# Kernel optimization log

Measured on AMD Instinct MI355X. Metric: run time of the kernel, lower is better.

The kernel has to match this reference:

```python
import jax, jax.numpy as jnp
import numpy as np

B, T, DIN, H = 8, 4096, 1024, 2048
INIT_SCALE = 0.1


def setup_inputs() -> dict:
    key = jax.random.key(0)
    ks = jax.random.split(key, 5)
    x = jax.random.normal(ks[0], (B, T, DIN), dtype=jnp.float32)
    Wi = jax.random.normal(ks[1], (H, DIN), dtype=jnp.float32) * INIT_SCALE
    Wg = jax.random.normal(ks[2], (H, DIN), dtype=jnp.float32) * INIT_SCALE
    Wo = jax.random.normal(ks[3], (DIN, H), dtype=jnp.float32) * INIT_SCALE
    log_a = jax.random.normal(ks[4], (H,), dtype=jnp.float32) * INIT_SCALE - 1.0
    bi = jnp.zeros((H,), dtype=jnp.float32)
    bg = jnp.zeros((H,), dtype=jnp.float32)
    bo = jnp.zeros((DIN,), dtype=jnp.float32)
    return {"x": x, "Wi": Wi, "bi": bi, "Wg": Wg, "bg": bg,
            "Wo": Wo, "bo": bo, "log_a": log_a}


def _lru_forward(x, Wi, bi, Wg, bg, Wo, bo, log_a):
    # u, gate: (B, T, H)
    u = jnp.einsum('btd,hd->bth', x, Wi) + bi
    gate = jax.nn.sigmoid(jnp.einsum('btd,hd->bth', x, Wg) + bg)
    a = jax.nn.sigmoid(log_a)  # (H,) diagonal recurrence coefficient

    # diagonal linear recurrence h_t = a*h_{t-1} + u_t, scanned over time
    def step(h, u_t):
        h = a * h + u_t
        return h, h

    u_tbh = jnp.swapaxes(u, 0, 1)  # (T, B, H)
    h0 = jnp.zeros((x.shape[0], log_a.shape[0]), dtype=x.dtype)
    _, h_seq = jax.lax.scan(step, h0, u_tbh)  # (T, B, H)
    h_seq = jnp.swapaxes(h_seq, 0, 1)  # (B, T, H)

    y = jnp.einsum('bth,dh->btd', h_seq * gate, Wo) + bo
    return y


def reference(x, Wi, bi, Wg, bg, Wo, bo, log_a):
    return _lru_forward(x, Wi, bi, Wg, bg, Wo, bo, log_a)
```

## Files before the change

### kernel.cpp

```cpp
#include <hip/hip_runtime.h>
#include <hip/hip_bf16.h>
#include <stdint.h>

using bf16 = __hip_bfloat16;

typedef short bf16x8 __attribute__((ext_vector_type(8)));
typedef float f32x4 __attribute__((ext_vector_type(4)));

#define BM 128
#define BN 128
#define BK 32

__device__ __forceinline__ float bf2f(bf16 x) { return __bfloat162float(x); }
__device__ __forceinline__ bf16 f2bf(float x) { return __float2bfloat16(x); }

__device__ __forceinline__ void async_load16(const bf16* gptr, bf16* lptr) {
    __builtin_amdgcn_global_load_lds(
        (const __attribute__((address_space(1))) void*)gptr,
        (__attribute__((address_space(3))) void*)lptr,
        16, 0, 0);
}

template <int MODE>
__global__ __launch_bounds__(256, 2) void gemm_bt(
    const bf16* __restrict__ A, const bf16* __restrict__ Bt,
    const float* __restrict__ bias, void* __restrict__ Cout,
    int M, int N, int K)
{
    __shared__ bf16 As[BM * BK];
    __shared__ bf16 Bs[BN * BK];

    const int tid  = threadIdx.x;
    const int wid  = tid >> 6;
    const int lane = tid & 63;

    const int m0 = blockIdx.y * BM;
    const int n0 = blockIdx.x * BN;
    const int wm = (wid >> 1) * 64;
    const int wn = (wid & 1) * 64;

    f32x4 acc[4][4];
#pragma unroll
    for (int i = 0; i < 4; ++i)
#pragma unroll
        for (int j = 0; j < 4; ++j)
            acc[i][j] = f32x4{0.f, 0.f, 0.f, 0.f};

    const int ar = lane >> 2;
    const int ac = (lane & 3) * 8;

    const bf16* Abase = A + (size_t)m0 * K;
    const bf16* Bbase = Bt + (size_t)n0 * K;

    const int frow = lane & 15;
    const int fk   = (lane >> 4) * 8;

    for (int k0 = 0; k0 < K; k0 += BK) {
        __syncthreads();
#pragma unroll
        for (int c = 0; c < 2; ++c) {
            const int chunk = wid + 4 * c;
            const int row = chunk * 16 + ar;
            async_load16(Abase + (size_t)row * K + (k0 + ac), &As[chunk * (16 * BK)]);
            async_load16(Bbase + (size_t)row * K + (k0 + ac), &Bs[chunk * (16 * BK)]);
        }
        __syncthreads();

        bf16x8 afrag[4], bfrag[4];
#pragma unroll
        for (int i = 0; i < 4; ++i) {
            afrag[i] = *(const bf16x8*)&As[(wm + 16 * i + frow) * BK + fk];
            bfrag[i] = *(const bf16x8*)&Bs[(wn + 16 * i + frow) * BK + fk];
        }
#pragma unroll
        for (int i = 0; i < 4; ++i)
#pragma unroll
            for (int j = 0; j < 4; ++j)
                acc[i][j] = __builtin_amdgcn_mfma_f32_16x16x32_bf16(
                    afrag[i], bfrag[j], acc[i][j], 0, 0, 0);
    }

    const int crow = (lane >> 4) * 4;
    const int ccol = lane & 15;
#pragma unroll
    for (int i = 0; i < 4; ++i) {
#pragma unroll
        for (int j = 0; j < 4; ++j) {
            const int col = n0 + wn + 16 * j + ccol;
            const float bv = bias[col];
#pragma unroll
            for (int r = 0; r < 4; ++r) {
                const int row = m0 + wm + 16 * i + crow + r;
                float v = acc[i][j][r] + bv;
                if constexpr (MODE == 1) v = 1.f / (1.f + __expf(-v));
                if constexpr (MODE == 2)
                    ((float*)Cout)[(size_t)row * N + col] = v;
                else
                    ((bf16*)Cout)[(size_t)row * N + col] = f2bf(v);
            }
        }
    }
}

#define SCAN_T 4096
#define SCAN_H 2048
#define SCAN_B 8
#define SCAN_L 512
#define SCAN_W 64

__global__ __launch_bounds__(256) void lru_scan(
    const bf16* __restrict__ u, bf16* gs, const float* __restrict__ asig)
{
    const int tid   = blockIdx.x * 256 + threadIdx.x;
    const int h     = tid & (SCAN_H - 1);
    const int rem   = tid >> 11;
    const int b     = rem & (SCAN_B - 1);
    const int chunk = rem >> 3;

    const float a = asig[h];
    const size_t base = (size_t)b * SCAN_T * SCAN_H + h;
    const bf16* up = u + base;
    bf16* gp = gs + base;

    const int t1 = chunk * SCAN_L;
    const int warm0 = (chunk == 0) ? 0 : SCAN_W;

    float hs = 0.f;
    for (int t = t1 - warm0; t < t1; t += 8) {
        float uv[8];
#pragma unroll
        for (int i = 0; i < 8; ++i) uv[i] = bf2f(up[(size_t)(t + i) * SCAN_H]);
#pragma unroll
        for (int i = 0; i < 8; ++i) hs = fmaf(a, hs, uv[i]);
    }
    for (int t = t1; t < t1 + SCAN_L; t += 8) {
        float uv[8], gv[8];
#pragma unroll
        for (int i = 0; i < 8; ++i) {
            uv[i] = bf2f(up[(size_t)(t + i) * SCAN_H]);
            gv[i] = bf2f(gp[(size_t)(t + i) * SCAN_H]);
        }
#pragma unroll
        for (int i = 0; i < 8; ++i) {
            hs = fmaf(a, hs, uv[i]);
            gp[(size_t)(t + i) * SCAN_H] = f2bf(hs * gv[i]);
        }
    }
}

__global__ void cvt_f32_bf16_x4(const float* __restrict__ in,
                                bf16* __restrict__ out, int n4)
{
    const int i = blockIdx.x * blockDim.x + threadIdx.x;
    if (i >= n4) return;
    const float4 v = ((const float4*)in)[i];
    bf16 h[4] __attribute__((aligned(8)));
    h[0] = f2bf(v.x); h[1] = f2bf(v.y); h[2] = f2bf(v.z); h[3] = f2bf(v.w);
    ((uint64_t*)out)[i] = *(const uint64_t*)h;
}

__global__ void sigmoid_vec(const float* __restrict__ in,
                            float* __restrict__ out, int n)
{
    const int i = blockIdx.x * blockDim.x + threadIdx.x;
    if (i < n) out[i] = 1.f / (1.f + __expf(-in[i]));
}

extern "C" void kernel_launch(void* const* d_in, const int* in_sizes, int n_in,
                              void* d_out, int out_size, void* d_ws, size_t ws_size,
                              hipStream_t stream)
{
    const float* x     = (const float*)d_in[0];
    const float* Wi    = (const float*)d_in[1];
    const float* bi    = (const float*)d_in[2];
    const float* Wg    = (const float*)d_in[3];
    const float* bg    = (const float*)d_in[4];
    const float* Wo    = (const float*)d_in[5];
    const float* bo    = (const float*)d_in[6];
    const float* log_a = (const float*)d_in[7];
    float* y = (float*)d_out;

    constexpr int Bc = 8, T = 4096, DIN = 1024, H = 2048;
    constexpr int M = Bc * T;

    char* ws = (char*)d_ws;
    size_t off = 0;
    auto alloc = [&](size_t bytes) -> void* {
        void* p = ws + off;
        off += (bytes + 255) & ~(size_t)255;
        return p;
    };
    bf16*  xb   = (bf16*)alloc((size_t)M * DIN * 2);
    bf16*  wib  = (bf16*)alloc((size_t)H * DIN * 2);
    bf16*  wgb  = (bf16*)alloc((size_t)H * DIN * 2);
    bf16*  wob  = (bf16*)alloc((size_t)DIN * H * 2);
    float* asig = (float*)alloc((size_t)H * 4);
    bf16*  u    = (bf16*)alloc((size_t)M * H * 2);
    bf16*  g    = (bf16*)alloc((size_t)M * H * 2);
    (void)ws_size; (void)in_sizes; (void)n_in; (void)out_size;

    {
        const int n4 = M * DIN / 4;
        cvt_f32_bf16_x4<<<(n4 + 255) / 256, 256, 0, stream>>>(x, xb, n4);
        const int w4 = H * DIN / 4;
        cvt_f32_bf16_x4<<<(w4 + 255) / 256, 256, 0, stream>>>(Wi, wib, w4);
        cvt_f32_bf16_x4<<<(w4 + 255) / 256, 256, 0, stream>>>(Wg, wgb, w4);
        cvt_f32_bf16_x4<<<(w4 + 255) / 256, 256, 0, stream>>>(Wo, wob, w4);
        sigmoid_vec<<<(H + 255) / 256, 256, 0, stream>>>(log_a, asig, H);
    }

    gemm_bt<0><<<dim3(H / BN, M / BM), 256, 0, stream>>>(xb, wib, bi, u, M, H, DIN);
    gemm_bt<1><<<dim3(H / BN, M / BM), 256, 0, stream>>>(xb, wgb, bg, g, M, H, DIN);

    lru_scan<<<(Bc * H * (T / SCAN_L)) / 256, 256, 0, stream>>>(u, g, asig);

    gemm_bt<2><<<dim3(DIN / BN, M / BM), 256, 0, stream>>>(g, wob, bo, y, M, DIN, H);
}
```

Baseline: 874.3 us.

## Replace GEMM with 256x256 double-buffered pipelined MFMA kernel

Replaces the simple 128x128 single-buffered GEMM with a 256x256-tile, 512-thread kernel. It double-buffers 64-wide K slices in LDS, interleaves async global-to-LDS loads with MFMA quadrants under fine-grained barriers and vmcnt waits, swizzles LDS rows to avoid bank conflicts, and remaps workgroups across XCDs for cache locality. The aim is to hide memory latency and raise MFMA utilisation in the three GEMMs that dominate runtime. In exchange it adds a complex hand-scheduled pipeline that assumes dimensions divisible by 256 and relies on precise wait counts.

```diff
diff --git a/kernel.cpp b/kernel.cpp
--- a/kernel.cpp
+++ b/kernel.cpp
@@ -6,10 +6,6 @@
 
 typedef short bf16x8 __attribute__((ext_vector_type(8)));
 typedef float f32x4 __attribute__((ext_vector_type(4)));
-
-#define BM 128
-#define BN 128
-#define BK 32
 
 __device__ __forceinline__ float bf2f(bf16 x) { return __bfloat162float(x); }
 __device__ __forceinline__ bf16 f2bf(float x) { return __float2bfloat16(x); }
@@ -21,76 +17,177 @@
         16, 0, 0);
 }
 
+__device__ __forceinline__ void wg_barrier() {
+    asm volatile("" ::: "memory");
+    __builtin_amdgcn_s_barrier();
+    asm volatile("" ::: "memory");
+}
+
+#define VMCNT(n) asm volatile("s_waitcnt vmcnt(" #n ")" ::: "memory")
+
 template <int MODE>
-__global__ __launch_bounds__(256, 2) void gemm_bt(
+__global__ __launch_bounds__(512, 2) void gemm256(
     const bf16* __restrict__ A, const bf16* __restrict__ Bt,
     const float* __restrict__ bias, void* __restrict__ Cout,
     int M, int N, int K)
 {
-    __shared__ bf16 As[BM * BK];
-    __shared__ bf16 Bs[BN * BK];
+    __shared__ bf16 lds[2 * 2 * 32 * 512];
 
     const int tid  = threadIdx.x;
     const int wid  = tid >> 6;
     const int lane = tid & 63;
-
-    const int m0 = blockIdx.y * BM;
-    const int n0 = blockIdx.x * BN;
-    const int wm = (wid >> 1) * 64;
-    const int wn = (wid & 1) * 64;
-
-    f32x4 acc[4][4];
-#pragma unroll
-    for (int i = 0; i < 4; ++i)
+    const int wm = wid >> 2;
+    const int wn = wid & 3;
+
+    const int nwg = gridDim.x;
+    const int q8 = nwg >> 3, r8 = nwg & 7;
+    const int xcd = blockIdx.x & 7, loc = blockIdx.x >> 3;
+    const int wgid = (xcd < r8 ? xcd * (q8 + 1) : r8 * (q8 + 1) + (xcd - r8) * q8) + loc;
+    const int ntn = N >> 8;
+    const int bx = wgid % ntn;
+    const int by = wgid / ntn;
+    const int m0 = by * 256;
+    const int n0 = bx * 256;
+
+    const bf16* Ablk = A  + (size_t)m0 * K;
+    const bf16* Bblk = Bt + (size_t)n0 * K;
+
+    const int frow = lane & 15;
+    const int fq   = lane >> 4;
+    const int roff = frow * 32 + ((fq ^ ((frow >> 1) & 3)) * 8);
+
+    const int swl  = lane ^ ((lane >> 3) & 3);
+    const int srow = swl >> 2;
+    const int scol = (swl & 3) * 8;
+
+    const int rgA = (wid & 3) + ((wid & 4) << 1);
+    const int rgB = (wid & 1) + ((wid & 2) << 1) + ((wid & 4) << 1);
+
+    auto stageA = [&](int buf, int k0, int q) {
+        const int rg = rgA + q * 4;
+        const bf16* g = Ablk + (size_t)(rg * 16 + srow) * K + (k0 + scol);
+        bf16* l = &lds[buf * 32768 + rg * 1024];
+        async_load16(g, l);
+        async_load16(g + 32, l + 512);
+    };
+    auto stageB = [&](int buf, int k0, int q) {
+        const int rg = rgB + q * 2;
+        const bf16* g = Bblk + (size_t)(rg * 16 + srow) * K + (k0 + scol);
+        bf16* l = &lds[buf * 32768 + 16384 + rg * 1024];
+        async_load16(g, l);
+        async_load16(g + 32, l + 512);
+    };
+
+    f32x4 acc[8][4];
+#pragma unroll
+    for (int i = 0; i < 8; ++i)
 #pragma unroll
         for (int j = 0; j < 4; ++j)
             acc[i][j] = f32x4{0.f, 0.f, 0.f, 0.f};
 
-    const int ar = lane >> 2;
-    const int ac = (lane & 3) * 8;
-
-    const bf16* Abase = A + (size_t)m0 * K;
-    const bf16* Bbase = Bt + (size_t)n0 * K;
-
-    const int frow = lane & 15;
-    const int fk   = (lane >> 4) * 8;
-
-    for (int k0 = 0; k0 < K; k0 += BK) {
-        __syncthreads();
-#pragma unroll
-        for (int c = 0; c < 2; ++c) {
-            const int chunk = wid + 4 * c;
-            const int row = chunk * 16 + ar;
-            async_load16(Abase + (size_t)row * K + (k0 + ac), &As[chunk * (16 * BK)]);
-            async_load16(Bbase + (size_t)row * K + (k0 + ac), &Bs[chunk * (16 * BK)]);
-        }
-        __syncthreads();
-
-        bf16x8 afrag[4], bfrag[4];
-#pragma unroll
-        for (int i = 0; i < 4; ++i) {
-            afrag[i] = *(const bf16x8*)&As[(wm + 16 * i + frow) * BK + fk];
-            bfrag[i] = *(const bf16x8*)&Bs[(wn + 16 * i + frow) * BK + fk];
-        }
+    bf16x8 af[4][2];
+    bf16x8 bfr[2][2][2];
+
+    auto LDA = [&](int buf, int ih) {
 #pragma unroll
         for (int i = 0; i < 4; ++i)
 #pragma unroll
-            for (int j = 0; j < 4; ++j)
-                acc[i][j] = __builtin_amdgcn_mfma_f32_16x16x32_bf16(
-                    afrag[i], bfrag[j], acc[i][j], 0, 0, 0);
-    }
-
-    const int crow = (lane >> 4) * 4;
-    const int ccol = lane & 15;
-#pragma unroll
-    for (int i = 0; i < 4; ++i) {
-#pragma unroll
-        for (int j = 0; j < 4; ++j) {
-            const int col = n0 + wn + 16 * j + ccol;
-            const float bv = bias[col];
+            for (int kk = 0; kk < 2; ++kk)
+                af[i][kk] = *(const bf16x8*)&lds[buf * 32768 +
+                    ((wm * 8 + ih * 4 + i) * 2 + kk) * 512 + roff];
+    };
+    auto LDB = [&](int buf, int jh) {
+#pragma unroll
+        for (int j = 0; j < 2; ++j)
+#pragma unroll
+            for (int kk = 0; kk < 2; ++kk)
+                bfr[jh][j][kk] = *(const bf16x8*)&lds[buf * 32768 + 16384 +
+                    ((wn * 4 + jh * 2 + j) * 2 + kk) * 512 + roff];
+    };
+    auto MFMAQ = [&](int ih, int jh) {
+        __builtin_amdgcn_s_setprio(1);
+#pragma unroll
+        for (int kk = 0; kk < 2; ++kk)
+#pragma unroll
+            for (int i = 0; i < 4; ++i)
+#pragma unroll
+                for (int j = 0; j < 2; ++j)
+                    acc[ih * 4 + i][jh * 2 + j] =
+                        __builtin_amdgcn_mfma_f32_16x16x32_bf16(
+                            af[i][kk], bfr[jh][j][kk],
+                            acc[ih * 4 + i][jh * 2 + j], 0, 0, 0);
+        __builtin_amdgcn_s_setprio(0);
+    };
+
+    stageA(0, 0, 0);
+    stageB(0, 0, 1);
+    stageA(0, 0, 1);
+    stageB(0, 0, 0);
+    stageA(1, 64, 0);
+    stageB(1, 64, 1);
+    VMCNT(4);
+    wg_barrier();
+
+    const int NT = K >> 6;
+    for (int t = 0; t < NT; t += 2) {
+        const int k1 = (t + 1) << 6;
+        const int k2 = (t + 2 < NT ? t + 2 : NT - 1) << 6;
+        const int k3 = (t + 3 < NT ? t + 3 : NT - 1) << 6;
+
+        LDA(0, 0); LDB(0, 0);
+        stageA(1, k1, 1);
+        wg_barrier();
+        MFMAQ(0, 0);
+        wg_barrier();
+        LDB(0, 1);
+        stageB(1, k1, 0);
+        wg_barrier();
+        MFMAQ(0, 1);
+        wg_barrier();
+        LDA(0, 1);
+        stageA(0, k2, 0);
+        wg_barrier();
+        MFMAQ(1, 1);
+        wg_barrier();
+        stageB(0, k2, 1);
+        wg_barrier();
+        MFMAQ(1, 0);
+        VMCNT(4);
+        wg_barrier();
+        LDA(1, 0); LDB(1, 0);
+        stageA(0, k2, 1);
+        wg_barrier();
+        MFMAQ(0, 0);
+        wg_barrier();
+        LDB(1, 1);
+        stageB(0, k2, 0);
+        wg_barrier();
+        MFMAQ(0, 1);
+        wg_barrier();
+        LDA(1, 1);
+        stageA(1, k3, 0);
+        wg_barrier();
+        MFMAQ(1, 1);
+        wg_barrier();
+        stageB(1, k3, 1);
+        wg_barrier();
+        MFMAQ(1, 0);
+        VMCNT(4);
+        wg_barrier();
+    }
+    asm volatile("s_waitcnt vmcnt(0)" ::: "memory");
+
+    const int crow = fq * 4;
+    const int ccol = frow;
+#pragma unroll
+    for (int j = 0; j < 4; ++j) {
+        const int col = n0 + wn * 64 + 16 * j + ccol;
+        const float bv = bias[col];
+#pragma unroll
+        for (int i = 0; i < 8; ++i) {
 #pragma unroll
             for (int r = 0; r < 4; ++r) {
-                const int row = m0 + wm + 16 * i + crow + r;
+                const int row = m0 + wm * 128 + 16 * i + crow + r;
                 float v = acc[i][j][r] + bv;
                 if constexpr (MODE == 1) v = 1.f / (1.f + __expf(-v));
                 if constexpr (MODE == 2)
@@ -209,10 +306,10 @@
         sigmoid_vec<<<(H + 255) / 256, 256, 0, stream>>>(log_a, asig, H);
     }
 
-    gemm_bt<0><<<dim3(H / BN, M / BM), 256, 0, stream>>>(xb, wib, bi, u, M, H, DIN);
-    gemm_bt<1><<<dim3(H / BN, M / BM), 256, 0, stream>>>(xb, wgb, bg, g, M, H, DIN);
+    gemm256<0><<<(M / 256) * (H / 256), 512, 0, stream>>>(xb, wib, bi, u, M, H, DIN);
+    gemm256<1><<<(M / 256) * (H / 256), 512, 0, stream>>>(xb, wgb, bg, g, M, H, DIN);
 
     lru_scan<<<(Bc * H * (T / SCAN_L)) / 256, 256, 0, stream>>>(u, g, asig);
 
-    gemm_bt<2><<<dim3(DIN / BN, M / BM), 256, 0, stream>>>(g, wob, bo, y, M, DIN, H);
-}
+    gemm256<2><<<(M / 256) * (DIN / 256), 512, 0, stream>>>(g, wob, bo, y, M, DIN, H);
+}
```

After: 763.0 us. 1.15x faster.
